# Kernel tuning notes

Hardware: AMD Instinct MI355X
Metric: run time of the kernel (lower is better)

The kernel has to match this reference:

```python
import jax, jax.numpy as jnp
import numpy as np

NPOINT = 1024
RADIUS = 1.0
NSAMPLE = 32
IN_CH = 64
COOR = 3


def _fps(xyz, npoint):
    # xyz: (B, N, 3) -> (B, npoint) farthest-point-sample indices.
    # Deterministic start at index 0 (torch version starts at a random index;
    # the algorithm/math is otherwise identical).
    B, N, _ = xyz.shape

    def step(carry, _):
        distance, farthest = carry
        centroid = jnp.take_along_axis(xyz, farthest[:, None, None], axis=1)  # (B,1,3)
        d = jnp.sum((xyz - centroid) ** 2, axis=-1)  # squared dist, (B,N)
        distance = jnp.minimum(distance, d)
        nxt = jnp.argmax(distance, axis=-1)
        return (distance, nxt), farthest

    init = (jnp.full((B, N), 1e10, dtype=xyz.dtype), jnp.zeros((B,), dtype=jnp.int32))
    _, idxs = jax.lax.scan(step, init, None, length=npoint)  # (npoint, B)
    return idxs.T  # (B, npoint)


def _sqdist(src, dst):
    # (B,M,C),(B,N,C) -> (B,M,N) squared distances
    return (jnp.sum(src ** 2, -1)[:, :, None]
            - 2.0 * jnp.einsum('bmc,bnc->bmn', src, dst)
            + jnp.sum(dst ** 2, -1)[:, None, :])


def _gather(points, idx):
    # points: (B,N,C); idx: (B,S) or (B,S,G)
    if idx.ndim == 2:
        return jnp.take_along_axis(points, idx[:, :, None], axis=1)
    return jax.vmap(lambda p, i: p[i])(points, idx)


def setup_inputs() -> dict:
    key = jax.random.key(0)
    k1, k2, k3 = jax.random.split(key, 3)
    B, N = 16, 8192
    points_coor = jax.random.normal(k1, (B, COOR, N), dtype=jnp.float32)
    points_fea = jax.random.normal(k2, (B, IN_CH, N), dtype=jnp.float32)
    # Conv2d(in_channel+coor_dim -> 2*in_channel, 1x1, bias=False) weight
    W = jax.random.normal(k3, (2 * IN_CH, IN_CH + COOR), dtype=jnp.float32) * 0.05
    return {"points_coor": points_coor, "points_fea": points_fea, "W": W}


def reference(points_coor, points_fea, W):
    xyz = jnp.transpose(points_coor, (0, 2, 1))  # (B,N,3)
    fea = jnp.transpose(points_fea, (0, 2, 1))   # (B,N,C)
    B, N, _ = xyz.shape

    # S: farthest point sampling
    fps_idx = _fps(xyz, NPOINT)          # (B,S)
    new_coor = _gather(xyz, fps_idx)     # (B,S,3)

    # G: hybrid KNN / ball query
    d = _sqdist(new_coor, xyz)                       # (B,S,N)
    neg_d, group_idx = jax.lax.top_k(-d, NSAMPLE)    # smallest distances
    dvals = -neg_d                                   # (B,S,G)
    group_idx = jnp.where(dvals > RADIUS ** 2, group_idx[:, :, :1], group_idx)

    grouped_coor = _gather(xyz, group_idx)                       # (B,S,G,3)
    grouped_coor = (grouped_coor - new_coor[:, :, None, :]) / RADIUS
    grouped_fea = _gather(fea, group_idx)                        # (B,S,G,C)
    grouped = jnp.concatenate([grouped_fea, grouped_coor], axis=-1)  # (B,S,G,C+3)

    # P: 1x1 conv (no bias, no norm — build_mlp never appends the norm) + ReLU + max-pool over group
    h = jax.nn.relu(jnp.einsum('bsgc,oc->bsgo', grouped, W))     # (B,S,G,2C)
    new_fea = jnp.max(h, axis=2)                                 # (B,S,2C)

    return (jnp.transpose(new_coor, (0, 2, 1)),    # (B,3,S)
            jnp.transpose(new_fea, (0, 2, 1)))     # (B,2C,S)
```

## Files before the change

kernel.cpp:

```cpp
#include <hip/hip_runtime.h>
#include <hip/hip_bf16.h>

#define BB 16
#define NN 8192
#define SS 1024
#define GG 32
#define SORT_R2 0xBF800000u

typedef float v2f __attribute__((ext_vector_type(2)));

__device__ __forceinline__ unsigned sortable(float f) {
    unsigned u = __float_as_uint(f);
    return u ^ ((unsigned)(((int)u) >> 31) | 0x80000000u);
}

template <int CTRL, int RM>
__device__ __forceinline__ float dpp_maxf(float v) {
    int i = __float_as_int(v);
    int p = __builtin_amdgcn_update_dpp(i, i, CTRL, RM, 0xF, false);
    return fmaxf(v, __int_as_float(p));
}

template <int CTRL, int RM>
__device__ __forceinline__ unsigned dpp_minu(unsigned v) {
    int p = __builtin_amdgcn_update_dpp((int)v, (int)v, CTRL, RM, 0xF, false);
    return min(v, (unsigned)p);
}

__device__ __forceinline__ float fmax3(float a, float b, float c) {
    return fmaxf(fmaxf(a, b), c);
}

__global__ __launch_bounds__(256) void k_pts(const float* __restrict__ coor,
                                             float4* __restrict__ pts4) {
    int i = blockIdx.x * 256 + threadIdx.x;
    int b = i >> 13, n = i & (NN - 1);
    const float* cb = coor + (long)b * 3 * NN;
    float x = cb[n], y = cb[NN + n], z = cb[2 * NN + n];
    float pn = __fadd_rn(__fadd_rn(__fmul_rn(x, x), __fmul_rn(y, y)), __fmul_rn(z, z));
    pts4[i] = make_float4(x, y, z, pn);
}

__global__ __launch_bounds__(256) void k_tr(const float* __restrict__ fea,
                                            float* __restrict__ feaT) {
    __shared__ float tile[64][65];
    int b = blockIdx.y, n0 = blockIdx.x * 64;
    int t = threadIdx.x;
    int nl = t & 63, cb = t >> 6;
#pragma unroll
    for (int i = 0; i < 16; i++) {
        int c = cb * 16 + i;
        tile[nl][c] = fea[((long)b * 64 + c) * NN + n0 + nl];
    }
    __syncthreads();
    int cl = t & 63, nb = t >> 6;
#pragma unroll
    for (int i = 0; i < 16; i++) {
        int n = nb * 16 + i;
        feaT[((long)b * NN + n0 + n) * 64 + cl] = tile[n][cl];
    }
}

__global__ __launch_bounds__(512) void k_fps(const float4* __restrict__ pts4,
                                             float4* __restrict__ qpts,
                                             float* __restrict__ out) {
#pragma clang fp contract(off)
    __shared__ float xs[NN], ys[NN], zs[NN];
    __shared__ int scur[SS];
    __shared__ unsigned long long gkey[3];
    int b = blockIdx.x;
    int t = threadIdx.x;
    const float4* P = pts4 + (long)b * NN;

    v2f px[8], py[8], pz[8], dist[8];
#pragma unroll
    for (int j = 0; j < 8; j++) {
        int p0 = t + (2 * j) * 512;
        int p1 = t + (2 * j + 1) * 512;
        float4 a = P[p0];
        float4 c = P[p1];
        px[j] = v2f{a.x, c.x};
        py[j] = v2f{a.y, c.y};
        pz[j] = v2f{a.z, c.z};
        dist[j] = v2f{1e10f, 1e10f};
        xs[p0] = a.x; ys[p0] = a.y; zs[p0] = a.z;
        xs[p1] = c.x; ys[p1] = c.y; zs[p1] = c.z;
    }
    if (t < 3) gkey[t] = 0ull;
    __syncthreads();

    int cur = 0;
    int par = 0;
    for (int s = 0; s < SS; s++) {
        float cx = xs[cur], cy = ys[cur], cz = zs[cur];
        int nxt = (par == 2) ? 0 : par + 1;
        if (t == 0) {
            scur[s] = cur;
            gkey[nxt] = 0ull;
        }
        v2f cx2 = v2f{cx, cx}, cy2 = v2f{cy, cy}, cz2 = v2f{cz, cz};
#pragma unroll
        for (int j = 0; j < 8; j++) {
            v2f dx = px[j] - cx2;
            v2f dy = py[j] - cy2;
            v2f dz = pz[j] - cz2;
            v2f xx = dx * dx;
            v2f yy = dy * dy;
            v2f zz = dz * dz;
            v2f sm = xx + yy;
            v2f d = sm + zz;
            dist[j] = __builtin_elementwise_min(dist[j], d);
        }
        v2f m01 = __builtin_elementwise_max(dist[0], dist[1]);
        v2f m23 = __builtin_elementwise_max(dist[2], dist[3]);
        v2f m45 = __builtin_elementwise_max(dist[4], dist[5]);
        v2f m67 = __builtin_elementwise_max(dist[6], dist[7]);
        v2f m03 = __builtin_elementwise_max(m01, m23);
        v2f m47 = __builtin_elementwise_max(m45, m67);
        v2f m07 = __builtin_elementwise_max(m03, m47);
        float bv = fmaxf(m07.x, m07.y);
        float wv = bv;
        wv = dpp_maxf<0x111, 0xF>(wv);
        wv = dpp_maxf<0x112, 0xF>(wv);
        wv = dpp_maxf<0x114, 0xF>(wv);
        wv = dpp_maxf<0x118, 0xF>(wv);
        wv = dpp_maxf<0x142, 0xA>(wv);
        wv = dpp_maxf<0x143, 0xC>(wv);
        float wm = __int_as_float(__builtin_amdgcn_readlane(__float_as_int(wv), 63));
        if (bv == wm) {
            int jj = 15;
#pragma unroll
            for (int j = 7; j >= 0; j--) {
                jj = (dist[j].y == bv) ? (2 * j + 1) : jj;
                jj = (dist[j].x == bv) ? (2 * j) : jj;
            }
            int p = t + jj * 512;
            unsigned long long key =
                ((unsigned long long)__float_as_uint(bv) << 32) | (unsigned)(8191 - p);
            atomicMax(&gkey[par], key);
        }
        __syncthreads();
        cur = 8191 - (int)((unsigned)(gkey[par] & 0xFFFFFFFFull));
        par = nxt;
    }
    __syncthreads();

#pragma unroll
    for (int s = t; s < SS; s += 512) {
        int c = scur[s];
        float cx = xs[c], cy = ys[c], cz = zs[c];
        out[(long)b * 3 * SS + s]          = cx;
        out[(long)b * 3 * SS + SS + s]     = cy;
        out[(long)b * 3 * SS + 2 * SS + s] = cz;
        float qn = __fadd_rn(__fadd_rn(__fmul_rn(cx, cx), __fmul_rn(cy, cy)),
                             __fmul_rn(cz, cz));
        qpts[(long)b * SS + s] = make_float4(cx, cy, cz, qn);
    }
}

#define SKEW(p) ((p) + ((p) >> 5))
__global__ __launch_bounds__(64) void k_knn(const float4* __restrict__ pts4,
                                            const float4* __restrict__ qpts,
                                            int* __restrict__ gidx) {
    __shared__ unsigned dk[NN + NN / 32];
    int Q = blockIdx.x;
    int b = Q >> 10;
    int l = threadIdx.x;
    float4 q = qpts[Q];
    const float4* P = pts4 + (long)b * NN;

    unsigned bmin = 0xFFFFFFFFu;
    int bpos = 0;
#pragma unroll 4
    for (int j = 0; j < 128; j++) {
        int p = j * 64 + l;
        float4 v = P[p];
        float dot = __fadd_rn(__fadd_rn(__fmul_rn(q.x, v.x), __fmul_rn(q.y, v.y)),
                              __fmul_rn(q.z, v.z));
        float d = __fadd_rn(__fsub_rn(q.w, __fmul_rn(2.0f, dot)), v.w);
        unsigned u = sortable(d);
        dk[SKEW(p)] = u;
        if (u < bmin) { bmin = u; bpos = p; }
    }
    __syncthreads();

    unsigned resv = 0;
    int resp = 0, pos0 = 0;
    for (int k = 0; k < GG; k++) {
        unsigned mv = bmin;
        mv = dpp_minu<0x111, 0xF>(mv);
        mv = dpp_minu<0x112, 0xF>(mv);
        mv = dpp_minu<0x114, 0xF>(mv);
        mv = dpp_minu<0x118, 0xF>(mv);
        mv = dpp_minu<0x142, 0xA>(mv);
        mv = dpp_minu<0x143, 0xC>(mv);
        unsigned wmin = (unsigned)__builtin_amdgcn_readlane((int)mv, 63);
        unsigned long long mask = __ballot(bmin == wmin);
        int wpos;
        if (__builtin_popcountll(mask) == 1) {
            int owner = __builtin_ctzll(mask);
            wpos = __builtin_amdgcn_readlane(bpos, owner);
        } else {
            unsigned long long kk =
                ((unsigned long long)bmin << 32) | (unsigned)bpos;
#pragma unroll
            for (int m = 1; m < 64; m <<= 1) {
                unsigned long long o = __shfl_xor(kk, m, 64);
                kk = (o < kk) ? o : kk;
            }
            wpos = (int)(kk & 0xFFFFFFFFull);
        }
        if (k == 0) pos0 = wpos;
        if (l == k) { resv = wmin; resp = wpos; }
        int own = wpos & 63;
        if (l == own) dk[SKEW(wpos)] = 0xFFFFFFFFu;
        __syncthreads();
        int p1 = l * 64 + own;
        int p2 = (l + 64) * 64 + own;
        unsigned v1 = dk[SKEW(p1)], v2 = dk[SKEW(p2)];
        bool c = v2 < v1;
        unsigned cv = c ? v2 : v1;
        int cp = c ? p2 : p1;
        unsigned cm = cv;
        cm = dpp_minu<0x111, 0xF>(cm);
        cm = dpp_minu<0x112, 0xF>(cm);
        cm = dpp_minu<0x114, 0xF>(cm);
        cm = dpp_minu<0x118, 0xF>(cm);
        cm = dpp_minu<0x142, 0xA>(cm);
        cm = dpp_minu<0x143, 0xC>(cm);
        unsigned colmin = (unsigned)__builtin_amdgcn_readlane((int)cm, 63);
        unsigned long long m2 = __ballot(cv == colmin);
        int colpos;
        if (__builtin_popcountll(m2) == 1) {
            colpos = __builtin_amdgcn_readlane(cp, __builtin_ctzll(m2));
        } else {
            unsigned long long kk =
                ((unsigned long long)cv << 32) | (unsigned)cp;
#pragma unroll
            for (int m = 1; m < 64; m <<= 1) {
                unsigned long long o = __shfl_xor(kk, m, 64);
                kk = (o < kk) ? o : kk;
            }
            colpos = (int)(kk & 0xFFFFFFFFull);
        }
        if (l == own) { bmin = colmin; bpos = colpos; }
        __syncthreads();
    }
    if (l < GG) {
        gidx[(long)Q * GG + l] = (resv > SORT_R2) ? pos0 : resp;
    }
}

__global__ __launch_bounds__(256, 2) void k_mlp(const float4* __restrict__ pts4,
                                                const float* __restrict__ feaT,
                                                const float4* __restrict__ qpts,
                                                const int* __restrict__ gidx,
                                                const float* __restrict__ W,
                                                float* __restrict__ out) {
    __shared__ float sm[8704];
    int t = threadIdx.x, l = t & 63, w = t >> 6;

    for (int i = t; i < 8576; i += 256) sm[i] = W[i];
    __syncthreads();
    float wa[68], wb[68];
#pragma unroll
    for (int c = 0; c < 68; c++) {
        wa[c] = (c < 67) ? sm[l * 67 + c] : 0.f;
        wb[c] = (c < 67) ? sm[(l + 64) * 67 + c] : 0.f;
    }
    __syncthreads();

    int Q = blockIdx.x * 4 + w;
    int b = Q >> 10, s = Q & 1023;
    float4 q = qpts[Q];
    const int* gi = gidx + (long)Q * GG;
    int base = w * 2176;

    if (l < 32) {
        int idx = gi[l];
        float4 p = pts4[(long)b * NN + idx];
        float4 rc = make_float4(__fsub_rn(p.x, q.x), __fsub_rn(p.y, q.y),
                                __fsub_rn(p.z, q.z), 0.f);
        *(float4*)&sm[base + l * 68 + 64] = rc;
    }
    {
        int g = l >> 1, half = l & 1;
        int idx = gi[g];
        const float4* f4 = (const float4*)(feaT + ((long)b * NN + idx) * 64);
#pragma unroll
        for (int k = 0; k < 8; k++) {
            *(float4*)&sm[base + g * 68 + half * 32 + k * 4] = f4[half * 8 + k];
        }
    }
    __syncthreads();

    float m0 = -1e30f, m1 = -1e30f;
#pragma unroll 2
    for (int g = 0; g < GG; g++) {
        float a0 = 0.f, a1 = 0.f;
#pragma unroll
        for (int c4 = 0; c4 < 17; c4++) {
            float4 gv = *(float4*)&sm[base + g * 68 + c4 * 4];
            a0 = fmaf(gv.x, wa[4 * c4 + 0], a0);
            a0 = fmaf(gv.y, wa[4 * c4 + 1], a0);
            a0 = fmaf(gv.z, wa[4 * c4 + 2], a0);
            a0 = fmaf(gv.w, wa[4 * c4 + 3], a0);
            a1 = fmaf(gv.x, wb[4 * c4 + 0], a1);
            a1 = fmaf(gv.y, wb[4 * c4 + 1], a1);
            a1 = fmaf(gv.z, wb[4 * c4 + 2], a1);
            a1 = fmaf(gv.w, wb[4 * c4 + 3], a1);
        }
        m0 = fmaxf(m0, a0);
        m1 = fmaxf(m1, a1);
    }
    out[49152 + ((long)b * 128 + l) * SS + s]      = fmaxf(m0, 0.f);
    out[49152 + ((long)b * 128 + l + 64) * SS + s] = fmaxf(m1, 0.f);
}

extern "C" void kernel_launch(void* const* d_in, const int* in_sizes, int n_in,
                              void* d_out, int out_size, void* d_ws, size_t ws_size,
                              hipStream_t stream) {
    const float* coor = (const float*)d_in[0];
    const float* fea  = (const float*)d_in[1];
    const float* Wm   = (const float*)d_in[2];
    float* out = (float*)d_out;

    char* ws = (char*)d_ws;
    float4* pts4 = (float4*)ws;
    float*  feaT = (float*)(ws + 2097152);
    float4* qpts = (float4*)(ws + 2097152 + 33554432);
    int*    gidx = (int*)(ws + 2097152 + 33554432 + 262144);

    k_pts<<<(BB * NN) / 256, 256, 0, stream>>>(coor, pts4);
    k_tr<<<dim3(NN / 64, BB), 256, 0, stream>>>(fea, feaT);
    k_fps<<<BB, 512, 0, stream>>>(pts4, qpts, out);
    k_knn<<<BB * SS, 64, 0, stream>>>(pts4, qpts, gidx);
    k_mlp<<<(BB * SS) / 4, 256, 0, stream>>>(pts4, feaT, qpts, gidx, Wm, out);
}
```

Before: 1.580 ms.

## Restructure FPS argmax to two-barrier shared reduction with 256 threads

FPS now runs 256 threads per block, each holding 32 points in registers instead of 16. The per-iteration argmax changes from one 64-bit atomicMax on a packed key to two steps: a shared-memory reduction of the four wave maxima, then an atomicMin on the index among threads holding the max. This removes the 64-bit LDS atomic and cuts the number of waves per barrier. It costs an extra __syncthreads per iteration, more register pressure, and twice the per-thread distance work on only 16 blocks.

```diff
diff --git a/kernel.cpp b/kernel.cpp
--- a/kernel.cpp
+++ b/kernel.cpp
@@ -61,22 +61,23 @@
     }
 }
 
-__global__ __launch_bounds__(512) void k_fps(const float4* __restrict__ pts4,
-                                             float4* __restrict__ qpts,
-                                             float* __restrict__ out) {
+__global__ __launch_bounds__(256, 1) void k_fps(const float4* __restrict__ pts4,
+                                                float4* __restrict__ qpts,
+                                                float* __restrict__ out) {
 #pragma clang fp contract(off)
     __shared__ float xs[NN], ys[NN], zs[NN];
     __shared__ int scur[SS];
-    __shared__ unsigned long long gkey[3];
+    __shared__ __align__(16) float redv[2][4];
+    __shared__ int sidx[2];
     int b = blockIdx.x;
     int t = threadIdx.x;
     const float4* P = pts4 + (long)b * NN;
 
-    v2f px[8], py[8], pz[8], dist[8];
-#pragma unroll
-    for (int j = 0; j < 8; j++) {
-        int p0 = t + (2 * j) * 512;
-        int p1 = t + (2 * j + 1) * 512;
+    v2f px[16], py[16], pz[16], dist[16];
+#pragma unroll
+    for (int j = 0; j < 16; j++) {
+        int p0 = t + (2 * j) * 256;
+        int p1 = t + (2 * j + 1) * 256;
         float4 a = P[p0];
         float4 c = P[p1];
         px[j] = v2f{a.x, c.x};
@@ -86,21 +87,17 @@
         xs[p0] = a.x; ys[p0] = a.y; zs[p0] = a.z;
         xs[p1] = c.x; ys[p1] = c.y; zs[p1] = c.z;
     }
-    if (t < 3) gkey[t] = 0ull;
+    if (t == 0) { sidx[0] = 0x7FFFFFFF; sidx[1] = 0x7FFFFFFF; }
     __syncthreads();
 
     int cur = 0;
-    int par = 0;
     for (int s = 0; s < SS; s++) {
+        int par = s & 1;
         float cx = xs[cur], cy = ys[cur], cz = zs[cur];
-        int nxt = (par == 2) ? 0 : par + 1;
-        if (t == 0) {
-            scur[s] = cur;
-            gkey[nxt] = 0ull;
-        }
+        if (t == 0) scur[s] = cur;
         v2f cx2 = v2f{cx, cx}, cy2 = v2f{cy, cy}, cz2 = v2f{cz, cz};
 #pragma unroll
-        for (int j = 0; j < 8; j++) {
+        for (int j = 0; j < 16; j++) {
             v2f dx = px[j] - cx2;
             v2f dy = py[j] - cy2;
             v2f dz = pz[j] - cz2;
@@ -111,13 +108,17 @@
             v2f d = sm + zz;
             dist[j] = __builtin_elementwise_min(dist[j], d);
         }
-        v2f m01 = __builtin_elementwise_max(dist[0], dist[1]);
-        v2f m23 = __builtin_elementwise_max(dist[2], dist[3]);
-        v2f m45 = __builtin_elementwise_max(dist[4], dist[5]);
-        v2f m67 = __builtin_elementwise_max(dist[6], dist[7]);
-        v2f m03 = __builtin_elementwise_max(m01, m23);
-        v2f m47 = __builtin_elementwise_max(m45, m67);
-        v2f m07 = __builtin_elementwise_max(m03, m47);
+        v2f m8[8];
+#pragma unroll
+        for (int i = 0; i < 8; i++)
+            m8[i] = __builtin_elementwise_max(dist[2 * i], dist[2 * i + 1]);
+        v2f m4a = __builtin_elementwise_max(m8[0], m8[1]);
+        v2f m4b = __builtin_elementwise_max(m8[2], m8[3]);
+        v2f m4c = __builtin_elementwise_max(m8[4], m8[5]);
+        v2f m4d = __builtin_elementwise_max(m8[6], m8[7]);
+        v2f m2a = __builtin_elementwise_max(m4a, m4b);
+        v2f m2b = __builtin_elementwise_max(m4c, m4d);
+        v2f m07 = __builtin_elementwise_max(m2a, m2b);
         float bv = fmaxf(m07.x, m07.y);
         float wv = bv;
         wv = dpp_maxf<0x111, 0xF>(wv);
@@ -126,27 +127,27 @@
         wv = dpp_maxf<0x118, 0xF>(wv);
         wv = dpp_maxf<0x142, 0xA>(wv);
         wv = dpp_maxf<0x143, 0xC>(wv);
-        float wm = __int_as_float(__builtin_amdgcn_readlane(__float_as_int(wv), 63));
-        if (bv == wm) {
-            int jj = 15;
-#pragma unroll
-            for (int j = 7; j >= 0; j--) {
-                jj = (dist[j].y == bv) ? (2 * j + 1) : jj;
-                jj = (dist[j].x == bv) ? (2 * j) : jj;
+        if ((t & 63) == 63) redv[par][t >> 6] = wv;
+        __syncthreads();
+        float4 r = *(const float4*)redv[par];
+        float gmax = fmaxf(fmaxf(r.x, r.y), fmaxf(r.z, r.w));
+        if (t == 0) sidx[1 - par] = 0x7FFFFFFF;
+        if (bv == gmax) {
+            int jj = 32;
+#pragma unroll
+            for (int j = 15; j >= 0; j--) {
+                jj = (dist[j].y == gmax) ? (2 * j + 1) : jj;
+                jj = (dist[j].x == gmax) ? (2 * j) : jj;
             }
-            int p = t + jj * 512;
-            unsigned long long key =
-                ((unsigned long long)__float_as_uint(bv) << 32) | (unsigned)(8191 - p);
-            atomicMax(&gkey[par], key);
+            atomicMin(&sidx[par], t + jj * 256);
         }
         __syncthreads();
-        cur = 8191 - (int)((unsigned)(gkey[par] & 0xFFFFFFFFull));
-        par = nxt;
-    }
-    __syncthreads();
-
-#pragma unroll
-    for (int s = t; s < SS; s += 512) {
+        cur = sidx[par];
+    }
+    __syncthreads();
+
+#pragma unroll
+    for (int s = t; s < SS; s += 256) {
         int c = scur[s];
         float cx = xs[c], cy = ys[c], cz = zs[c];
         out[(long)b * 3 * SS + s]          = cx;
@@ -333,7 +334,7 @@
 
     k_pts<<<(BB * NN) / 256, 256, 0, stream>>>(coor, pts4);
     k_tr<<<dim3(NN / 64, BB), 256, 0, stream>>>(fea, feaT);
-    k_fps<<<BB, 512, 0, stream>>>(pts4, qpts, out);
+    k_fps<<<BB, 256, 0, stream>>>(pts4, qpts, out);
     k_knn<<<BB * SS, 64, 0, stream>>>(pts4, qpts, gidx);
     k_mlp<<<(BB * SS) / 4, 256, 0, stream>>>(pts4, feaT, qpts, gidx, Wm, out);
 }
```

After: 1.595 ms. About the same (+1.0%).

## Fuse KNN and MLP kernels and simplify FPS argmax reduction

Applied to the files above, without the earlier changes.

Merges the KNN grouping kernel with the MLP kernel so the 32 neighbor indices stay in shared memory, and reuses the KNN distance buffer for the gathered features. This removes the gidx round trip through global memory and one launch. Weights are now loaded per lane straight from global memory instead of through shared memory. The FPS loop swaps its 64-bit atomicMax keyed on value plus index for a two-stage reduction: per-wave maxima go to shared memory, then lanes holding the max do an atomicMin on the index. This adds one extra barrier per iteration and keeps the lowest-index tie-break.

```diff
diff --git a/kernel.cpp b/kernel.cpp
--- a/kernel.cpp
+++ b/kernel.cpp
@@ -67,7 +67,8 @@
 #pragma clang fp contract(off)
     __shared__ float xs[NN], ys[NN], zs[NN];
     __shared__ int scur[SS];
-    __shared__ unsigned long long gkey[3];
+    __shared__ __align__(16) float redv[2][8];
+    __shared__ int sidx[2];
     int b = blockIdx.x;
     int t = threadIdx.x;
     const float4* P = pts4 + (long)b * NN;
@@ -86,18 +87,14 @@
         xs[p0] = a.x; ys[p0] = a.y; zs[p0] = a.z;
         xs[p1] = c.x; ys[p1] = c.y; zs[p1] = c.z;
     }
-    if (t < 3) gkey[t] = 0ull;
+    if (t == 0) { sidx[0] = 0x7FFFFFFF; sidx[1] = 0x7FFFFFFF; }
     __syncthreads();
 
     int cur = 0;
-    int par = 0;
     for (int s = 0; s < SS; s++) {
+        int par = s & 1;
         float cx = xs[cur], cy = ys[cur], cz = zs[cur];
-        int nxt = (par == 2) ? 0 : par + 1;
-        if (t == 0) {
-            scur[s] = cur;
-            gkey[nxt] = 0ull;
-        }
+        if (t == 0) scur[s] = cur;
         v2f cx2 = v2f{cx, cx}, cy2 = v2f{cy, cy}, cz2 = v2f{cz, cz};
 #pragma unroll
         for (int j = 0; j < 8; j++) {
@@ -126,22 +123,24 @@
         wv = dpp_maxf<0x118, 0xF>(wv);
         wv = dpp_maxf<0x142, 0xA>(wv);
         wv = dpp_maxf<0x143, 0xC>(wv);
-        float wm = __int_as_float(__builtin_amdgcn_readlane(__float_as_int(wv), 63));
-        if (bv == wm) {
-            int jj = 15;
+        if ((t & 63) == 63) redv[par][t >> 6] = wv;
+        __syncthreads();
+        float4 r0 = *(const float4*)redv[par];
+        float4 r1 = *(const float4*)(redv[par] + 4);
+        float gmax = fmaxf(fmax3(r0.x, r0.y, r0.z),
+                           fmax3(r0.w, fmax3(r1.x, r1.y, r1.z), r1.w));
+        if (t == 0) sidx[1 - par] = 0x7FFFFFFF;
+        if (bv == gmax) {
+            int jj = 16;
 #pragma unroll
             for (int j = 7; j >= 0; j--) {
-                jj = (dist[j].y == bv) ? (2 * j + 1) : jj;
-                jj = (dist[j].x == bv) ? (2 * j) : jj;
+                jj = (dist[j].y == gmax) ? (2 * j + 1) : jj;
+                jj = (dist[j].x == gmax) ? (2 * j) : jj;
             }
-            int p = t + jj * 512;
-            unsigned long long key =
-                ((unsigned long long)__float_as_uint(bv) << 32) | (unsigned)(8191 - p);
-            atomicMax(&gkey[par], key);
+            atomicMin(&sidx[par], t + jj * 512);
         }
         __syncthreads();
-        cur = 8191 - (int)((unsigned)(gkey[par] & 0xFFFFFFFFull));
-        par = nxt;
+        cur = sidx[par];
     }
     __syncthreads();
 
@@ -159,19 +158,24 @@
 }
 
 #define SKEW(p) ((p) + ((p) >> 5))
-__global__ __launch_bounds__(64) void k_knn(const float4* __restrict__ pts4,
-                                            const float4* __restrict__ qpts,
-                                            int* __restrict__ gidx) {
-    __shared__ unsigned dk[NN + NN / 32];
+__global__ __launch_bounds__(64) void k_knn_mlp(const float4* __restrict__ pts4,
+                                                const float* __restrict__ feaT,
+                                                const float4* __restrict__ qpts,
+                                                const float* __restrict__ W,
+                                                float* __restrict__ out) {
+    __shared__ __align__(16) unsigned dk[NN + NN / 32];
+    __shared__ int sidxs[GG];
+    float* grouped = (float*)dk;
+
     int Q = blockIdx.x;
-    int b = Q >> 10;
+    int b = Q >> 10, s = Q & 1023;
     int l = threadIdx.x;
     float4 q = qpts[Q];
     const float4* P = pts4 + (long)b * NN;
 
     unsigned bmin = 0xFFFFFFFFu;
     int bpos = 0;
-#pragma unroll 4
+#pragma unroll 8
     for (int j = 0; j < 128; j++) {
         int p = j * 64 + l;
         float4 v = P[p];
@@ -183,6 +187,17 @@
         if (u < bmin) { bmin = u; bpos = p; }
     }
     __syncthreads();
+
+    float wa[68], wb[68];
+    {
+        const float* Wr = W + l * 67;
+#pragma unroll
+        for (int c = 0; c < 67; c++) {
+            wa[c] = Wr[c];
+            wb[c] = Wr[64 * 67 + c];
+        }
+        wa[67] = 0.f; wb[67] = 0.f;
+    }
 
     unsigned resv = 0;
     int resp = 0, pos0 = 0;
@@ -246,50 +261,24 @@
         if (l == own) { bmin = colmin; bpos = colpos; }
         __syncthreads();
     }
-    if (l < GG) {
-        gidx[(long)Q * GG + l] = (resv > SORT_R2) ? pos0 : resp;
-    }
-}
-
-__global__ __launch_bounds__(256, 2) void k_mlp(const float4* __restrict__ pts4,
-                                                const float* __restrict__ feaT,
-                                                const float4* __restrict__ qpts,
-                                                const int* __restrict__ gidx,
-                                                const float* __restrict__ W,
-                                                float* __restrict__ out) {
-    __shared__ float sm[8704];
-    int t = threadIdx.x, l = t & 63, w = t >> 6;
-
-    for (int i = t; i < 8576; i += 256) sm[i] = W[i];
-    __syncthreads();
-    float wa[68], wb[68];
-#pragma unroll
-    for (int c = 0; c < 68; c++) {
-        wa[c] = (c < 67) ? sm[l * 67 + c] : 0.f;
-        wb[c] = (c < 67) ? sm[(l + 64) * 67 + c] : 0.f;
-    }
-    __syncthreads();
-
-    int Q = blockIdx.x * 4 + w;
-    int b = Q >> 10, s = Q & 1023;
-    float4 q = qpts[Q];
-    const int* gi = gidx + (long)Q * GG;
-    int base = w * 2176;
+
+    if (l < GG) sidxs[l] = (resv > SORT_R2) ? pos0 : resp;
+    __syncthreads();
 
     if (l < 32) {
-        int idx = gi[l];
+        int idx = sidxs[l];
         float4 p = pts4[(long)b * NN + idx];
         float4 rc = make_float4(__fsub_rn(p.x, q.x), __fsub_rn(p.y, q.y),
                                 __fsub_rn(p.z, q.z), 0.f);
-        *(float4*)&sm[base + l * 68 + 64] = rc;
+        *(float4*)&grouped[l * 68 + 64] = rc;
     }
     {
         int g = l >> 1, half = l & 1;
-        int idx = gi[g];
+        int idx = sidxs[g];
         const float4* f4 = (const float4*)(feaT + ((long)b * NN + idx) * 64);
 #pragma unroll
-        for (int k = 0; k < 8; k++) {
-            *(float4*)&sm[base + g * 68 + half * 32 + k * 4] = f4[half * 8 + k];
+        for (int k4 = 0; k4 < 8; k4++) {
+            *(float4*)&grouped[g * 68 + half * 32 + k4 * 4] = f4[half * 8 + k4];
         }
     }
     __syncthreads();
@@ -300,7 +289,7 @@
         float a0 = 0.f, a1 = 0.f;
 #pragma unroll
         for (int c4 = 0; c4 < 17; c4++) {
-            float4 gv = *(float4*)&sm[base + g * 68 + c4 * 4];
+            float4 gv = *(float4*)&grouped[g * 68 + c4 * 4];
             a0 = fmaf(gv.x, wa[4 * c4 + 0], a0);
             a0 = fmaf(gv.y, wa[4 * c4 + 1], a0);
             a0 = fmaf(gv.z, wa[4 * c4 + 2], a0);
@@ -329,11 +318,9 @@
     float4* pts4 = (float4*)ws;
     float*  feaT = (float*)(ws + 2097152);
     float4* qpts = (float4*)(ws + 2097152 + 33554432);
-    int*    gidx = (int*)(ws + 2097152 + 33554432 + 262144);
 
     k_pts<<<(BB * NN) / 256, 256, 0, stream>>>(coor, pts4);
     k_tr<<<dim3(NN / 64, BB), 256, 0, stream>>>(fea, feaT);
     k_fps<<<BB, 512, 0, stream>>>(pts4, qpts, out);
-    k_knn<<<BB * SS, 64, 0, stream>>>(pts4, qpts, gidx);
-    k_mlp<<<(BB * SS) / 4, 256, 0, stream>>>(pts4, feaT, qpts, gidx, Wm, out);
-}
+    k_knn_mlp<<<BB * SS, 64, 0, stream>>>(pts4, feaT, qpts, Wm, out);
+}
```

After: 1.501 ms. 5.0% less time.
